# Kernel tuning notes

Measured on AMD Instinct MI355X. Metric: run time of the kernel, lower is better.

Reference implementation:

```python
import jax, jax.numpy as jnp
import numpy as np
from itertools import permutations

NUM_LAYERS = 3
K = 5  # fixed node degree -> every Hungarian sub-problem is 5x5
# one-hot permutation tensor: P1H[p, r, c] = 1 iff permutation p assigns row r -> col c
PERMS = np.array(list(permutations(range(K))), dtype=np.int32)          # [120, K]
P1H = (PERMS[:, :, None] == np.arange(K)[None, None, :]).astype(np.float32)  # [120, K, K]


def _mlp(x, W1, b1, W2, b2):
    # 2-layer MLP with ReLU (repo's MLP(in, hid, out, 2))
    return jax.nn.relu(x @ W1 + b1) @ W2 + b2


def _sinkhorn(src, itera):
    s = jax.nn.softmax(src, axis=1)  # row-max subtraction is built in
    for i in range(itera):
        s = s / jnp.sum(s, axis=i % 2, keepdims=True)
    return jnp.nan_to_num(s)


def _masked_softmax(src):
    s1 = jnp.nan_to_num(jax.nn.softmax(src, axis=1))
    s2 = jnp.nan_to_num(jax.nn.softmax(src, axis=0))
    return (s1 + s2) * 0.5


def setup_inputs() -> dict:
    key = jax.random.key(0)
    ks = jax.random.split(key, 12)
    n1 = n2 = 1024
    hid = 64
    adj1 = jax.random.randint(ks[0], (n1, K), 0, n1)
    adj2 = jax.random.randint(ks[1], (n2, K), 0, n2)
    # adjacency matrices consistent with the neighbor lists
    G1 = jnp.zeros((n1, n1), jnp.float32).at[jnp.arange(n1)[:, None], adj1].set(1.0)
    G2 = jnp.zeros((n2, n2), jnp.float32).at[jnp.arange(n2)[:, None], adj2].set(1.0)
    s = 0.1
    return {
        'G1': G1, 'G2': G2, 'adj1': adj1, 'adj2': adj2,
        'ro_W1': jax.random.normal(ks[2], (NUM_LAYERS, 1, hid), jnp.float32) * s,
        'ro_b1': jax.random.normal(ks[3], (NUM_LAYERS, hid), jnp.float32) * s,
        'ro_W2': jax.random.normal(ks[4], (NUM_LAYERS, hid, 1), jnp.float32) * s,
        'ro_b2': jax.random.normal(ks[5], (NUM_LAYERS, 1), jnp.float32) * s,
        'fin_W1': jax.random.normal(ks[6], (1, hid), jnp.float32) * s,
        'fin_b1': jax.random.normal(ks[7], (hid,), jnp.float32) * s,
        'fin_W2': jax.random.normal(ks[8], (hid, 1), jnp.float32) * s,
        'fin_b2': jax.random.normal(ks[9], (1,), jnp.float32) * s,
    }


def reference(G1, G2, adj1, adj2, ro_W1, ro_b1, ro_W2, ro_b2, fin_W1, fin_b1, fin_W2, fin_b2):
    n1 = G1.shape[0]
    n2 = G2.shape[0]
    d1 = jnp.sum(G1, axis=1)
    d2 = jnp.sum(G2, axis=1)
    ttheta = jnp.mean(d1)
    # S[i, j, 0] = -|d1[i] - d2[j]|
    S = -jnp.abs(d1[:, None] - d2[None, :])[..., None]  # [n1, n2, 1]
    p1h = jnp.asarray(P1H)
    for li in range(NUM_LAYERS):
        Wn = _sinkhorn(_mlp(S / ttheta, ro_W1[li], ro_b1[li], ro_W2[li], ro_b2[li]).squeeze(-1), 5)
        W = jnp.log(Wn * (n1 * 1.5))
        W = jnp.where(jnp.isneginf(W), jnp.float32(-1e12), W)
        W = jnp.where(jnp.isposinf(W), jnp.float32(1e12), W)
        Wd = jax.lax.stop_gradient(W)  # matches W.detach().numpy()
        # small[a, b, r, c] = Wd[adj1[a, r], adj2[b, c]]  -> [n1, n2, K, K]
        small = jnp.transpose(Wd[adj1][:, :, adj2], (0, 2, 1, 3))
        # exact linear_sum_assignment(-small): maximize sum over the K! permutations
        scores = jnp.einsum('abrc,prc->abp', small, p1h)  # [n1, n2, 120]
        X1 = jnp.max(scores, axis=-1)                      # [n1, n2]
        S = X1[..., None]
    out = _masked_softmax(_mlp(S, fin_W1, fin_b1, fin_W2, fin_b2).squeeze(-1))
    return out
```

## Files before the change

kernel.cpp:

```cpp
#include <hip/hip_runtime.h>
#include <math.h>

#define N 1024
#define NB 256
#define KD 5
#define SL 8
#define NT 126
#define MAGIC 0x13572468
#define FSTRIDE 32
#define FREGION (NB * FSTRIDE + FSTRIDE)


__device__ __forceinline__ float load_sc(const float* p){
  return __hip_atomic_load(p, __ATOMIC_RELAXED, __HIP_MEMORY_SCOPE_AGENT);
}
__device__ __forceinline__ void store_sc(float* p, float v){
  __hip_atomic_store(p, v, __ATOMIC_RELAXED, __HIP_MEMORY_SCOPE_AGENT);
}
__device__ __forceinline__ int load_sci(const int* p){
  return __hip_atomic_load(p, __ATOMIC_RELAXED, __HIP_MEMORY_SCOPE_AGENT);
}
__device__ __forceinline__ void store_sci(int* p, int v){
  __hip_atomic_store(p, v, __ATOMIC_RELAXED, __HIP_MEMORY_SCOPE_AGENT);
}

__device__ __forceinline__ void gbarS(int* flg){
  __builtin_amdgcn_s_waitcnt(0);
  __syncthreads();
  const int t = threadIdx.x, B = blockIdx.x;
  int* go = flg + NB * FSTRIDE;
  if (B == 0){
    if (t > 0 && t < NB){
      while (load_sci(&flg[t * FSTRIDE]) != MAGIC) __builtin_amdgcn_s_sleep(1);
    }
    __syncthreads();
    if (t == 0) store_sci(go, MAGIC);
  } else {
    if (t == 0){
      store_sci(&flg[B * FSTRIDE], MAGIC);
      while (load_sci(go) != MAGIC) __builtin_amdgcn_s_sleep(1);
    }
    __syncthreads();
  }
}

__device__ __forceinline__ float wred_sum(float v){
#pragma unroll
  for (int off = 32; off > 0; off >>= 1) v += __shfl_down(v, off);
  return v;
}
__device__ __forceinline__ void bsum4(float v[4], float* s64){
  float w0 = wred_sum(v[0]), w1 = wred_sum(v[1]), w2 = wred_sum(v[2]), w3 = wred_sum(v[3]);
  __syncthreads();
  int wv = threadIdx.x >> 6;
  if ((threadIdx.x & 63) == 0){ s64[wv*4] = w0; s64[wv*4+1] = w1; s64[wv*4+2] = w2; s64[wv*4+3] = w3; }
  __syncthreads();
  float r0 = 0.f, r1 = 0.f, r2 = 0.f, r3 = 0.f;
#pragma unroll
  for (int i = 0; i < 16; ++i){ r0 += s64[i*4]; r1 += s64[i*4+1]; r2 += s64[i*4+2]; r3 += s64[i*4+3]; }
  v[0] = r0; v[1] = r1; v[2] = r2; v[3] = r3;
}

__device__ __forceinline__ int distinct5(const int* v){
  int c = 0;
#pragma unroll
  for (int r = 0; r < KD; ++r){
    bool dup = false;
#pragma unroll
    for (int s = 0; s < r; ++s) dup = dup || (v[s] == v[r]);
    c += dup ? 0 : 1;
  }
  return c;
}
__device__ __forceinline__ void sort5(int* s){
#pragma unroll
  for (int i = 0; i < 4; ++i)
#pragma unroll
    for (int j = 0; j < 4 - i; ++j){
      int a = s[j], b = s[j+1];
      s[j] = min(a, b); s[j+1] = max(a, b);
    }
}
__device__ __forceinline__ int msrank(const int* c5){
  const int C_[6][5] = { {0,0,0,0,0},
                         {1,1,1,1,1},
                         {1,2,3,4,5},
                         {1,3,6,10,15},
                         {1,4,10,20,35},
                         {1,5,15,35,70} };
  int rank = 0, prev = 0;
#pragma unroll
  for (int i = 0; i < 5; ++i){
    for (int v = prev; v < c5[i]; ++v) rank += C_[5 - v][4 - i];
    prev = c5[i];
  }
  return rank;
}

#define DP5(ACCESS, OUT) {                                        \
  float f[32]; f[0] = 0.f;                                        \
  _Pragma("unroll")                                               \
  for (int r = 0; r < KD; ++r){                                   \
    float tr[KD];                                                 \
    _Pragma("unroll")                                             \
    for (int c = 0; c < KD; ++c) tr[c] = (ACCESS);                \
    _Pragma("unroll")                                             \
    for (int m = 1; m < 32; ++m){                                 \
      if (__popc(m) == r + 1){                                    \
        float dpb = 0.f; bool dpi = true;                         \
        _Pragma("unroll")                                         \
        for (int c = 0; c < KD; ++c)                              \
          if (m & (1 << c)){                                      \
            float dpv = f[m ^ (1 << c)] + tr[c];                  \
            dpb = dpi ? dpv : fmaxf(dpb, dpv);                    \
            dpi = false;                                          \
          }                                                       \
        f[m] = dpb;                                               \
      }                                                           \
    }                                                             \
  }                                                               \
  OUT = f[31];                                                    \
}

__device__ __forceinline__ void pwl_build(int t,
    const float* __restrict__ w1g, const float* __restrict__ b1g,
    const float* __restrict__ w2g, const float* __restrict__ b2g,
    float* ux, float* udA, float* udB,
    float* xss, float* dAs, float* dBs,
    float* Atb, float* Btb, float* sA0B0)
{
  if (t < 64){
    float w1 = w1g[t], bb = b1g[t], w2v = w2g[t];
    float xk, sdA, sdB, a0t = 0.f, b0t = 0.f;
    if (w1 != 0.f){
      xk = -bb / w1;
      float dA = w1 * w2v, dB = bb * w2v;
      if (w1 > 0.f){ sdA = dA;  sdB = dB; }
      else         { sdA = -dA; sdB = -dB; a0t = dA; b0t = dB; }
    } else {
      xk = 3.0e38f; sdA = 0.f; sdB = 0.f;
      b0t = fmaxf(bb, 0.f) * w2v;
    }
    ux[t] = xk; udA[t] = sdA; udB[t] = sdB;
    float A0 = wred_sum(a0t);
    float B0 = wred_sum(b0t);
    if (t == 0){ sA0B0[0] = A0; sA0B0[1] = B0 + b2g[0]; }
  }
  __syncthreads();
  if (t < 64){
    float xk = ux[t]; int rank = 0;
    for (int j = 0; j < 64; ++j){
      float xj = ux[j];
      rank += (xj < xk || (xj == xk && j < t)) ? 1 : 0;
    }
    xss[rank] = ux[t]; dAs[rank] = udA[t]; dBs[rank] = udB[t];
  }
  __syncthreads();
  if (t < 65){
    float sa = sA0B0[0], sb = sA0B0[1];
    for (int r = 0; r < t; ++r){ sa += dAs[r]; sb += dBs[r]; }
    Atb[t] = sa; Btb[t] = sb;
  }
  __syncthreads();
}

__global__ __launch_bounds__(1024) void
kFused(const int* __restrict__ adj1, const int* __restrict__ adj2,
       const float* __restrict__ roW1, const float* __restrict__ roB1,
       const float* __restrict__ roW2, const float* __restrict__ roB2,
       const float* __restrict__ fW1, const float* __restrict__ fB1,
       const float* __restrict__ fW2, const float* __restrict__ fB2,
       float* __restrict__ tY1g,
       float* __restrict__ C1B, float* __restrict__ C2B, float* __restrict__ C3B,
       float* __restrict__ CFB, float* __restrict__ Rg,
       float* __restrict__ outp,
       int* __restrict__ flg)
{
  __shared__ __align__(16) char uS[20 * N * 4 + N * 4];
  float* tY1 = (float*)uS;
  float (*rows20)[N] = (float (*)[N])uS;
  float* lc = (float*)(uS + 20 * N * 4);
  __shared__ unsigned char t2c[NT][5];
  __shared__ unsigned char sg1[N], sg2[N];
  __shared__ unsigned short st1[N], st2[N];
  __shared__ int h1[8], h2[8];
  __shared__ int cnt1T[NT], cnt2T[NT];
  __shared__ float A1[NT], B1[NT];
  __shared__ float sY0[25], slR0[5], slC0[5], stt2[2];
  __shared__ float slR1[NT], slC1[NT];
  __shared__ float vq[NT], vC[NT], vqi[NT], vCi[NT];
  __shared__ float s64[64], sAv[4];
  __shared__ float ux[64], udA[64], udB[64], xss[64], dAs[64], dBs[64];
  __shared__ float Atb[65], Btb[65], sA0B0[2];
  __shared__ float xs3[64], A3t[65], B3t[65];

  const int t = threadIdx.x, B = blockIdx.x;
  const float L1536 = logf(1536.0f);

  if (t < 8){ h1[t] = 0; h2[t] = 0; }
  if (t < NT){ cnt1T[t] = 0; cnt2T[t] = 0; }
#pragma unroll 1
  for (int key = t; key < 3125; key += 1024){
    int d[5]; int k2 = key;
#pragma unroll
    for (int i = 0; i < 5; ++i){ d[i] = k2 % 5; k2 /= 5; }
    if (d[0] <= d[1] && d[1] <= d[2] && d[2] <= d[3] && d[3] <= d[4]){
      int r = msrank(d);
#pragma unroll
      for (int i = 0; i < 5; ++i) t2c[r][i] = (unsigned char)d[i];
    }
  }
  int a2[KD], a1v[KD];
#pragma unroll
  for (int c = 0; c < KD; ++c) a2[c] = adj2[t * KD + c];
#pragma unroll
  for (int r = 0; r < KD; ++r) a1v[r] = adj1[t * KD + r];
  {
    int c2 = distinct5(a2) - 1, c1 = distinct5(a1v) - 1;
    sg2[t] = (unsigned char)c2; sg1[t] = (unsigned char)c1;
    atomicAdd(&h2[c2], 1);
    atomicAdd(&h1[c1], 1);
  }
  __syncthreads();

  {
    int c5[KD];
#pragma unroll
    for (int r = 0; r < KD; ++r) c5[r] = sg1[a1v[r]];
    sort5(c5);
    int ty = msrank(c5);
    st1[t] = (unsigned short)ty; atomicAdd(&cnt1T[ty], 1);
  }
  {
    int c5[KD];
#pragma unroll
    for (int c = 0; c < KD; ++c) c5[c] = sg2[a2[c]];
    sort5(c5);
    int ty = msrank(c5);
    st2[t] = (unsigned short)ty; atomicAdd(&cnt2T[ty], 1);
  }

  if (t < 64){
    float cnt1[5], cnt2[5];
#pragma unroll
    for (int g = 0; g < 5; ++g){ cnt1[g] = (float)h1[g]; cnt2[g] = (float)h2[g]; }
    float tt = 0.f;
#pragma unroll
    for (int g = 0; g < 5; ++g) tt += (float)(g + 1) * cnt1[g];
    tt *= (1.0f / 1024.0f);
    float tab[5];
#pragma unroll 1
    for (int i = 0; i < 5; ++i){
      float x = -(float)i / tt;
      float acc = roB2[0];
      for (int k = 0; k < 64; ++k){
        float hh = fmaxf(fmaf(x, roW1[k], roB1[k]), 0.f);
        acc = fmaf(hh, roW2[k], acc);
      }
      tab[i] = acc;
    }
    float Ee[5][5];
#pragma unroll
    for (int g = 0; g < 5; ++g)
#pragma unroll
      for (int h = 0; h < 5; ++h) Ee[g][h] = expf(tab[abs(g - h)]);
    float q0[5], C1c[5], q1[5], C2c[5], q2[5], C3c[5];
#pragma unroll
    for (int g = 0; g < 5; ++g){
      float s = 0.f;
#pragma unroll
      for (int h = 0; h < 5; ++h) s += cnt2[h] * Ee[g][h];
      q0[g] = s;
    }
#pragma unroll
    for (int h = 0; h < 5; ++h){
      float s = 0.f;
#pragma unroll
      for (int g = 0; g < 5; ++g) s += cnt1[g] * Ee[g][h] / q0[g];
      C1c[h] = s;
    }
#pragma unroll
    for (int g = 0; g < 5; ++g){
      float s = 0.f;
#pragma unroll
      for (int h = 0; h < 5; ++h) s += cnt2[h] * Ee[g][h] / C1c[h];
      q1[g] = s;
    }
#pragma unroll
    for (int h = 0; h < 5; ++h){
      float s = 0.f;
#pragma unroll
      for (int g = 0; g < 5; ++g) s += cnt1[g] * Ee[g][h] / q1[g];
      C2c[h] = s;
    }
#pragma unroll
    for (int g = 0; g < 5; ++g){
      float s = 0.f;
#pragma unroll
      for (int h = 0; h < 5; ++h) s += cnt2[h] * Ee[g][h] / C2c[h];
      q2[g] = s;
    }
#pragma unroll
    for (int h = 0; h < 5; ++h){
      float s = 0.f;
#pragma unroll
      for (int g = 0; g < 5; ++g) s += cnt1[g] * Ee[g][h] / q2[g];
      C3c[h] = s;
    }
    if (t == 0){
#pragma unroll
      for (int g = 0; g < 5; ++g){
#pragma unroll
        for (int h = 0; h < 5; ++h) sY0[g * 5 + h] = tab[abs(g - h)];
        slR0[g] = -logf(q2[g]);
        slC0[g] = logf(C3c[g]);
      }
      stt2[0] = tt;
    }
  } else if (t < 128){
    int l = t - 64;
    const float* w1g = roW1 + 64;
    const float* b1g = roB1 + 64;
    const float* w2g = roW2 + 64;
    const float* b2g = roB2 + 1;
    float w1 = w1g[l], bb = b1g[l], w2v = w2g[l];
    float xk, sdA, sdB, a0t = 0.f, b0t = 0.f;
    if (w1 != 0.f){
      xk = -bb / w1;
      float dA = w1 * w2v, dB = bb * w2v;
      if (w1 > 0.f){ sdA = dA;  sdB = dB; }
      else         { sdA = -dA; sdB = -dB; a0t = dA; b0t = dB; }
    } else {
      xk = 3.0e38f; sdA = 0.f; sdB = 0.f;
      b0t = fmaxf(bb, 0.f) * w2v;
    }
    ux[l] = xk; udA[l] = sdA; udB[l] = sdB;
    float A0 = wred_sum(a0t);
    float B0 = wred_sum(b0t);
    if (l == 0){ sA0B0[0] = A0; sA0B0[1] = B0 + b2g[0]; }
  }
  __syncthreads();

  if (t < 64){
    float xk = ux[t]; int rank = 0;
    for (int j = 0; j < 64; ++j){
      float xj = ux[j];
      rank += (xj < xk || (xj == xk && j < t)) ? 1 : 0;
    }
    xss[rank] = ux[t]; dAs[rank] = udA[t]; dBs[rank] = udB[t];
  } else if (t >= 256 && t < 256 + NT){
    int ty = t - 256;
    float sa = 5.0f * L1536, sb = 0.f;
#pragma unroll
    for (int i = 0; i < KD; ++i){
      int cl = t2c[ty][i];
      sa += slR0[cl];
      sb -= slC0[cl];
    }
    A1[ty] = sa; B1[ty] = sb;
  }
  __syncthreads();
  if (t < 65){
    float sa = sA0B0[0], sb = sA0B0[1];
    for (int r = 0; r < t; ++r){ sa += dAs[r]; sb += dBs[r]; }
    Atb[t] = sa; Btb[t] = sb;
  }
  __syncthreads();

  const float tt = stt2[0];
  if (t < 63){
    int e = B + 256 * t;
    if (e < NT * NT){
      int tau = e / NT, ups = e - tau * NT;
      const unsigned char* G = t2c[tau];
      const unsigned char* H = t2c[ups];
      float D;
      DP5(sY0[(int)G[r] * 5 + (int)H[c]], D);
      float x = (A1[tau] + B1[ups] + D) / tt;
      int seg = 0;
#pragma unroll
      for (int s = 64; s; s >>= 1)
        if (seg + s <= 64 && xss[seg + s - 1] <= x) seg += s;
      store_sc(&tY1g[e], fmaf(Atb[seg], x, Btb[seg]));
    }
  }

  pwl_build(t, fW1, fB1, fW2, fB2,
            ux, udA, udB, xs3, dAs, dBs, A3t, B3t, sA0B0);

  gbarS(flg + 0 * FREGION);

  float rv[16];
#pragma unroll
  for (int i = 0; i < 16; ++i){
    int e = t + 1024 * i;
    if (e < NT * NT) rv[i] = load_sc(&tY1g[e]);
  }
#pragma unroll
  for (int i = 0; i < 16; ++i){
    int e = t + 1024 * i;
    if (e < NT * NT) tY1[e] = rv[i];
  }

  pwl_build(t, roW1 + 128, roB1 + 128, roW2 + 128, roB2 + 2,
            ux, udA, udB, xss, dAs, dBs, Atb, Btb, sA0B0);

  int stc[KD];
#pragma unroll
  for (int c = 0; c < KD; ++c) stc[c] = st2[a2[c]];
  float D2[4];
#pragma unroll 1
  for (int rr = 0; rr < 4; ++rr){
    int str_[KD];
#pragma unroll
    for (int r = 0; r < KD; ++r) str_[r] = st1[adj1[(4 * B + rr) * KD + r]];
    float D;
    DP5(tY1[str_[r] * NT + stc[c]], D);
    D2[rr] = D;
  }
  __syncthreads();
#pragma unroll
  for (int i = 0; i < 16; ++i){
    int e = t + 1024 * i;
    if (e < NT * NT) tY1[e] = expf(rv[i]);
  }
  __syncthreads();

  {
    int g = t >> 3, j = t & 7;
    float Er[16], Ec[16];
    if (g < NT){
#pragma unroll
      for (int i = 0; i < 16; ++i){
        int u = j + 8 * i;
        if (u < NT){
          Er[i] = (float)cnt2T[u] * tY1[g * NT + u];
          Ec[i] = (float)cnt1T[u] * tY1[u * NT + g];
        } else { Er[i] = 0.f; Ec[i] = 0.f; }
      }
    }
    if (g < NT){
      float acc = 0.f;
#pragma unroll
      for (int i = 0; i < 16; ++i){ int u = j + 8 * i; if (u < NT) acc += Er[i]; }
      acc += __shfl_down(acc, 4, 8); acc += __shfl_down(acc, 2, 8); acc += __shfl_down(acc, 1, 8);
      if (j == 0){ vq[g] = acc; vqi[g] = 1.0f / acc; }
    }
    __syncthreads();
    if (g < NT){
      float acc = 0.f;
#pragma unroll
      for (int i = 0; i < 16; ++i){ int u = j + 8 * i; if (u < NT) acc += Ec[i] * vqi[u]; }
      acc += __shfl_down(acc, 4, 8); acc += __shfl_down(acc, 2, 8); acc += __shfl_down(acc, 1, 8);
      if (j == 0){ vC[g] = acc; vCi[g] = 1.0f / acc; }
    }
    __syncthreads();
    if (g < NT){
      float acc = 0.f;
#pragma unroll
      for (int i = 0; i < 16; ++i){ int u = j + 8 * i; if (u < NT) acc += Er[i] * vCi[u]; }
      acc += __shfl_down(acc, 4, 8); acc += __shfl_down(acc, 2, 8); acc += __shfl_down(acc, 1, 8);
      if (j == 0){ vq[g] = acc; vqi[g] = 1.0f / acc; }
    }
    __syncthreads();
    if (g < NT){
      float acc = 0.f;
#pragma unroll
      for (int i = 0; i < 16; ++i){ int u = j + 8 * i; if (u < NT) acc += Ec[i] * vqi[u]; }
      acc += __shfl_down(acc, 4, 8); acc += __shfl_down(acc, 2, 8); acc += __shfl_down(acc, 1, 8);
      if (j == 0){ vC[g] = acc; vCi[g] = 1.0f / acc; }
    }
    __syncthreads();
    if (g < NT){
      float acc = 0.f;
#pragma unroll
      for (int i = 0; i < 16; ++i){ int u = j + 8 * i; if (u < NT) acc += Er[i] * vCi[u]; }
      acc += __shfl_down(acc, 4, 8); acc += __shfl_down(acc, 2, 8); acc += __shfl_down(acc, 1, 8);
      if (j == 0){ vq[g] = acc; vqi[g] = 1.0f / acc; }
    }
    __syncthreads();
    if (g < NT){
      float acc = 0.f;
#pragma unroll
      for (int i = 0; i < 16; ++i){ int u = j + 8 * i; if (u < NT) acc += Ec[i] * vqi[u]; }
      acc += __shfl_down(acc, 4, 8); acc += __shfl_down(acc, 2, 8); acc += __shfl_down(acc, 1, 8);
      if (j == 0) vC[g] = acc;
    }
    __syncthreads();
  }
  if (t < NT){ slR1[t] = -logf(vq[t]); slC1[t] = logf(vC[t]); }
  __syncthreads();

  if (t < 4){
    int a = 4 * B + t;
    float s = 5.0f * L1536;
#pragma unroll
    for (int r = 0; r < KD; ++r) s += slR1[st1[adj1[a * KD + r]]];
    sAv[t] = s;
  }
  float Bv2 = 0.f;
#pragma unroll
  for (int c = 0; c < KD; ++c) Bv2 -= slC1[stc[c]];
  __syncthreads();

  float y2[4];
#pragma unroll
  for (int rr = 0; rr < 4; ++rr){
    float x = (sAv[rr] + Bv2 + D2[rr]) / tt;
    int seg = 0;
#pragma unroll
    for (int s = 64; s; s >>= 1)
      if (seg + s <= 64 && xss[seg + s - 1] <= x) seg += s;
    y2[rr] = fmaf(Atb[seg], x, Btb[seg]);
  }
  float E[4], q4[4];
#pragma unroll
  for (int r = 0; r < 4; ++r){ E[r] = expf(y2[r]); q4[r] = E[r]; }
  bsum4(q4, s64);
  {
    float cp = 0.f;
#pragma unroll
    for (int r = 0; r < 4; ++r){
      store_sc(&outp[(size_t)(4 * B + r) * N + t], y2[r]);
      cp += E[r] / q4[r];
    }
    atomicAdd(&C1B[(size_t)(B & (SL - 1)) * N + t], cp);
  }

  gbarS(flg + 1 * FREGION);

  float rv20[20];
#pragma unroll
  for (int k = 0; k < 20; ++k){
    int src = adj1[(4 * B + (k / 5)) * KD + (k % 5)];
    rv20[k] = load_sc(&outp[(size_t)src * N + t]);
  }

  {
    float C = 0.f;
#pragma unroll
    for (int k = 0; k < SL; ++k) C += load_sc(&C1B[(size_t)k * N + t]);
    float iC = 1.0f / C;
#pragma unroll
    for (int r = 0; r < 4; ++r) q4[r] = E[r] * iC;
    bsum4(q4, s64);
    float cp = 0.f;
#pragma unroll
    for (int r = 0; r < 4; ++r) cp += E[r] / q4[r];
    atomicAdd(&C2B[(size_t)(B & (SL - 1)) * N + t], cp);
  }

#pragma unroll
  for (int k = 0; k < 20; ++k) rows20[k][t] = rv20[k];
  __syncthreads();
  float D3[4];
#pragma unroll 1
  for (int rr = 0; rr < 4; ++rr){
    float D;
    DP5(rows20[rr * 5 + r][a2[c]], D);
    D3[rr] = D;
  }

  gbarS(flg + 2 * FREGION);
  {
    float C = 0.f;
#pragma unroll
    for (int k = 0; k < SL; ++k) C += load_sc(&C2B[(size_t)k * N + t]);
    float iC = 1.0f / C;
#pragma unroll
    for (int r = 0; r < 4; ++r) q4[r] = E[r] * iC;
    bsum4(q4, s64);
    float cp = 0.f;
#pragma unroll
    for (int r = 0; r < 4; ++r) cp += E[r] / q4[r];
    if (t < 4) store_sc(&Rg[4 * B + t], 1.0f / q4[t]);
    atomicAdd(&C3B[(size_t)(B & (SL - 1)) * N + t], cp);
  }

  gbarS(flg + 3 * FREGION);
  {
    float C = 0.f;
#pragma unroll
    for (int k = 0; k < SL; ++k) C += load_sc(&C3B[(size_t)k * N + t]);
    lc[t] = logf(C);
  }
  if (t >= 64 && t < 68){
    int a = 4 * B + (t - 64);
    float s = 5.0f * logf(1536.0f);
#pragma unroll
    for (int r = 0; r < KD; ++r) s += logf(load_sc(&Rg[adj1[a * KD + r]]));
    sAv[t - 64] = s;
  }
  __syncthreads();

  float Bvl = 0.f;
#pragma unroll
  for (int c = 0; c < KD; ++c) Bvl -= lc[a2[c]];

  float y[4];
#pragma unroll
  for (int rr = 0; rr < 4; ++rr){
    float x = sAv[rr] + Bvl + D3[rr];
    int seg = 0;
#pragma unroll
    for (int s = 64; s; s >>= 1)
      if (seg + s <= 64 && xs3[seg + s - 1] <= x) seg += s;
    y[rr] = fmaf(A3t[seg], x, B3t[seg]);
  }

  float e4[4];
#pragma unroll
  for (int r = 0; r < 4; ++r){ e4[r] = expf(y[r]); q4[r] = e4[r]; }
  bsum4(q4, s64);

  {
    float cp = 0.f;
#pragma unroll
    for (int r = 0; r < 4; ++r) cp += e4[r];
    atomicAdd(&CFB[(size_t)(B & (SL - 1)) * N + t], cp);
  }

  gbarS(flg + 4 * FREGION);
  float CF = 0.f;
#pragma unroll
  for (int k = 0; k < SL; ++k) CF += load_sc(&CFB[(size_t)k * N + t]);
  float iCF = 1.0f / CF;
#pragma unroll
  for (int r = 0; r < 4; ++r){
    float v = 0.5f * e4[r] * (1.0f / q4[r] + iCF);
    outp[(size_t)(4 * B + r) * N + t] = v;
  }
}

extern "C" void kernel_launch(void* const* d_in, const int* in_sizes, int n_in,
                              void* d_out, int out_size, void* d_ws, size_t ws_size,
                              hipStream_t stream){
  (void)in_sizes; (void)n_in; (void)out_size; (void)ws_size;
  const int*   adj1 = (const int*)d_in[2];
  const int*   adj2 = (const int*)d_in[3];
  const float* roW1 = (const float*)d_in[4];
  const float* roB1 = (const float*)d_in[5];
  const float* roW2 = (const float*)d_in[6];
  const float* roB2 = (const float*)d_in[7];
  const float* fW1  = (const float*)d_in[8];
  const float* fB1  = (const float*)d_in[9];
  const float* fW2  = (const float*)d_in[10];
  const float* fB2  = (const float*)d_in[11];
  float* out = (float*)d_out;

  float* Pp   = (float*)d_ws;
  float* Rg   = Pp + (size_t)4 * SL * N;
  float* tY1g = Rg + N;
  int*   flg  = (int*)(tY1g + NT * NT);

  kFused<<<NB, 1024, 0, stream>>>(adj1, adj2, roW1, roB1, roW2, roB2,
                                  fW1, fB1, fW2, fB2,
                                  tY1g,
                                  Pp + (size_t)0 * SL * N, Pp + (size_t)1 * SL * N,
                                  Pp + (size_t)2 * SL * N, Pp + (size_t)3 * SL * N,
                                  Rg, out, flg);
}
```

Measured before the change: 150.3 us.

## Split grid barrier into arrive/wait phases and pad shared table rows

Splits the software grid barrier into separate arrive and wait halves so that independent work (the PWL table builds, the rows20 dot products and the reciprocal of q4) runs between signalling arrival and waiting for the release. This is meant to hide barrier latency behind useful work. The 126-wide shared table is also padded to a 136-float row stride to reduce LDS bank conflicts on the column-wise reads, which adds an explicit __syncthreads after the table fill. The overlap is only safe if the work placed between arrive and wait does not read data produced by other blocks in that phase.

```diff
diff --git a/kernel.cpp b/kernel.cpp
--- a/kernel.cpp
+++ b/kernel.cpp
@@ -6,6 +6,7 @@
 #define KD 5
 #define SL 8
 #define NT 126
+#define NTP 136
 #define MAGIC 0x13572468
 #define FSTRIDE 32
 #define FREGION (NB * FSTRIDE + FSTRIDE)
@@ -24,9 +25,13 @@
   __hip_atomic_store(p, v, __ATOMIC_RELAXED, __HIP_MEMORY_SCOPE_AGENT);
 }
 
-__device__ __forceinline__ void gbarS(int* flg){
+__device__ __forceinline__ void gbar_arrive(int* flg){
   __builtin_amdgcn_s_waitcnt(0);
   __syncthreads();
+  if (blockIdx.x != 0 && threadIdx.x == 0)
+    store_sci(&flg[blockIdx.x * FSTRIDE], MAGIC);
+}
+__device__ __forceinline__ void gbar_wait(int* flg){
   const int t = threadIdx.x, B = blockIdx.x;
   int* go = flg + NB * FSTRIDE;
   if (B == 0){
@@ -37,12 +42,12 @@
     if (t == 0) store_sci(go, MAGIC);
   } else {
     if (t == 0){
-      store_sci(&flg[B * FSTRIDE], MAGIC);
       while (load_sci(go) != MAGIC) __builtin_amdgcn_s_sleep(1);
     }
     __syncthreads();
   }
 }
+__device__ __forceinline__ void gbarS(int* flg){ gbar_arrive(flg); gbar_wait(flg); }
 
 __device__ __forceinline__ float wred_sum(float v){
 #pragma unroll
@@ -385,25 +390,29 @@
     }
   }
 
+  gbar_arrive(flg + 0 * FREGION);
   pwl_build(t, fW1, fB1, fW2, fB2,
             ux, udA, udB, xs3, dAs, dBs, A3t, B3t, sA0B0);
-
-  gbarS(flg + 0 * FREGION);
+  pwl_build(t, roW1 + 128, roB1 + 128, roW2 + 128, roB2 + 2,
+            ux, udA, udB, xss, dAs, dBs, Atb, Btb, sA0B0);
+  gbar_wait(flg + 0 * FREGION);
 
   float rv[16];
+  int lidx[16];
 #pragma unroll
   for (int i = 0; i < 16; ++i){
     int e = t + 1024 * i;
-    if (e < NT * NT) rv[i] = load_sc(&tY1g[e]);
+    if (e < NT * NT){
+      rv[i] = load_sc(&tY1g[e]);
+      lidx[i] = e + (NTP - NT) * (e / NT);
+    }
   }
 #pragma unroll
   for (int i = 0; i < 16; ++i){
     int e = t + 1024 * i;
-    if (e < NT * NT) tY1[e] = rv[i];
-  }
-
-  pwl_build(t, roW1 + 128, roB1 + 128, roW2 + 128, roB2 + 2,
-            ux, udA, udB, xss, dAs, dBs, Atb, Btb, sA0B0);
+    if (e < NT * NT) tY1[lidx[i]] = rv[i];
+  }
+  __syncthreads();
 
   int stc[KD];
 #pragma unroll
@@ -415,14 +424,14 @@
 #pragma unroll
     for (int r = 0; r < KD; ++r) str_[r] = st1[adj1[(4 * B + rr) * KD + r]];
     float D;
-    DP5(tY1[str_[r] * NT + stc[c]], D);
+    DP5(tY1[str_[r] * NTP + stc[c]], D);
     D2[rr] = D;
   }
   __syncthreads();
 #pragma unroll
   for (int i = 0; i < 16; ++i){
     int e = t + 1024 * i;
-    if (e < NT * NT) tY1[e] = expf(rv[i]);
+    if (e < NT * NT) tY1[lidx[i]] = expf(rv[i]);
   }
   __syncthreads();
 
@@ -434,8 +443,8 @@
       for (int i = 0; i < 16; ++i){
         int u = j + 8 * i;
         if (u < NT){
-          Er[i] = (float)cnt2T[u] * tY1[g * NT + u];
-          Ec[i] = (float)cnt1T[u] * tY1[u * NT + g];
+          Er[i] = (float)cnt2T[u] * tY1[g * NTP + u];
+          Ec[i] = (float)cnt1T[u] * tY1[u * NTP + g];
         } else { Er[i] = 0.f; Ec[i] = 0.f; }
       }
     }
@@ -550,6 +559,7 @@
     atomicAdd(&C2B[(size_t)(B & (SL - 1)) * N + t], cp);
   }
 
+  gbar_arrive(flg + 2 * FREGION);
 #pragma unroll
   for (int k = 0; k < 20; ++k) rows20[k][t] = rv20[k];
   __syncthreads();
@@ -560,8 +570,8 @@
     DP5(rows20[rr * 5 + r][a2[c]], D);
     D3[rr] = D;
   }
-
-  gbarS(flg + 2 * FREGION);
+  gbar_wait(flg + 2 * FREGION);
+
   {
     float C = 0.f;
 #pragma unroll
@@ -620,14 +630,19 @@
     atomicAdd(&CFB[(size_t)(B & (SL - 1)) * N + t], cp);
   }
 
-  gbarS(flg + 4 * FREGION);
+  gbar_arrive(flg + 4 * FREGION);
+  float iq[4];
+#pragma unroll
+  for (int r = 0; r < 4; ++r) iq[r] = 1.0f / q4[r];
+  gbar_wait(flg + 4 * FREGION);
+
   float CF = 0.f;
 #pragma unroll
   for (int k = 0; k < SL; ++k) CF += load_sc(&CFB[(size_t)k * N + t]);
   float iCF = 1.0f / CF;
 #pragma unroll
   for (int r = 0; r < 4; ++r){
-    float v = 0.5f * e4[r] * (1.0f / q4[r] + iCF);
+    float v = 0.5f * e4[r] * (iq[r] + iCF);
     outp[(size_t)(4 * B + r) * N + t] = v;
   }
 }
```

After: 146.3 us. 2.7% less time.
